# Kernel tuning notes

Hardware: AMD Instinct MI355X
Metric: run time of the kernel (lower is better)

## Reference

```python
import jax, jax.numpy as jnp
import numpy as np

LAMBDA = 0.5
WINDOW = 2
NUM_SCALES = 2
EPS = 1e-5


def setup_inputs() -> dict:
    key = jax.random.key(0)
    ks = jax.random.split(key, 9)
    N, C, T, Vw = 32, 96, 300, 50
    V = 25
    out_c = 192
    return {
        "x": jax.random.normal(ks[0], (N, C, T, Vw), jnp.float32),
        "xx": jax.random.normal(ks[1], (N, 3, 300, V), jnp.float32),
        "A_res": jax.random.normal(ks[2], (Vw, Vw), jnp.float32) * 1e-6,
        "W": jax.random.normal(ks[3], (out_c, NUM_SCALES * C), jnp.float32) * 0.05,
        "b": jax.random.normal(ks[4], (out_c,), jnp.float32) * 0.01,
        "gamma": jnp.ones((out_c,), jnp.float32),
        "beta": jnp.zeros((out_c,), jnp.float32),
        "running_mean": jax.random.normal(ks[5], (out_c,), jnp.float32) * 0.01,
        "running_var": jax.random.uniform(ks[6], (out_c,), jnp.float32, 0.5, 1.5),
    }


def reference(x, xx, A_res, W, b, gamma, beta, running_mean, running_var):
    # xx: (N, 3, 300, V) -> (N, T=300, V, C=3)
    xxp = jnp.transpose(xx, (0, 2, 3, 1))
    # pairwise squared L2 distances (norm then squared in exp == sum of squares)
    diff = xxp[:, :, :, None, :] - xxp[:, :, None, :, :]      # (N,T,V,V,3)
    dists2 = jnp.sum(diff * diff, axis=-1)                     # (N,T,V,V)
    A_dsg = jnp.exp(-dists2 / LAMBDA)
    # conv3d with (1,1,300,1,1) kernel of 1/300 == mean over the 300 frames
    A_t = jnp.mean(A_dsg, axis=1)                              # (N,V,V)
    # per-sample symmetric normalization D^-1/2 A D^-1/2
    deg = jnp.sum(A_t, axis=-1)                                # (N,V)
    dinv = deg ** -0.5
    A_norm = A_t * dinv[:, :, None] * dinv[:, None, :]
    # kron-style repeat to spatial-temporal graph (N, V*window, V*window)
    A_large = jnp.tile(A_norm, (1, WINDOW, WINDOW))
    A = A_large + A_res                                        # (N,Vw,Vw)
    # conv2d with (1,N,1,1) kernel of 1/N == mean over the batch
    A_scale = jnp.mean(A, axis=0)                              # (Vw,Vw)
    # graph conv
    agg = jnp.einsum('vu,nctu->nctv', A_scale, x)              # (N,C,T,Vw)
    N, C, T, Vw = x.shape
    Vs = Vw // NUM_SCALES
    agg = agg.reshape(N, C, T, NUM_SCALES, Vs)
    agg = jnp.transpose(agg, (0, 3, 1, 2, 4)).reshape(N, NUM_SCALES * C, T, Vs)
    # MLP: 1x1 conv + BN (activation='linear')
    out = jnp.einsum('oc,nctv->notv', W, agg) + b[None, :, None, None]
    scale = gamma * jax.lax.rsqrt(running_var + EPS)
    out = out * scale[None, :, None, None] + (beta - running_mean * scale)[None, :, None, None]
    return jax.nn.relu(out)
```

## Files before the change

### kernel.cpp

```cpp
#include <hip/hip_runtime.h>
#include <hip/hip_bf16.h>

typedef __attribute__((ext_vector_type(8))) short short8;
typedef __attribute__((ext_vector_type(4))) short short4v;
typedef __attribute__((ext_vector_type(4))) float f32x4;
typedef __attribute__((ext_vector_type(2))) float f32x2;

__device__ __forceinline__ unsigned short f2bf(float f) {
    unsigned int u = __builtin_bit_cast(unsigned int, f);
    u += 0x7fffu + ((u >> 16) & 1u);
    return (unsigned short)(u >> 16);
}
__device__ __forceinline__ short4v cvt4(float a, float b, float c, float d) {
    union { __hip_bfloat162 h[2]; short4v s; } u;
    u.h[0] = __float22bfloat162_rn(make_float2(a, b));
    u.h[1] = __float22bfloat162_rn(make_float2(c, d));
    return u.s;
}

__global__ void kA(const float* __restrict__ xx, float* __restrict__ At_part) {
    __shared__ float xs3[3][60][25];
    const int tc = blockIdx.x, n = blockIdx.y;
    const int tid = threadIdx.x;
    const float* base = xx + (size_t)n * 22500 + tc * 1500;
    for (int idx = tid; idx < 4500; idx += 256) {
        int ch = idx / 1500, rt = idx % 1500;
        xs3[ch][rt / 25][rt % 25] = base[ch * 7500 + rt];
    }
    __syncthreads();
    for (int p = tid; p < 625; p += 256) {
        int v = p / 25, u = p % 25;
        float s = 0.f;
        for (int t = 0; t < 60; ++t) {
            float dx = xs3[0][t][v] - xs3[0][t][u];
            float dy = xs3[1][t][v] - xs3[1][t][u];
            float dz = xs3[2][t][v] - xs3[2][t][u];
            s += __expf(-2.f * (dx * dx + dy * dy + dz * dz));
        }
        At_part[(size_t)(n * 5 + tc) * 625 + p] = s;
    }
}

__global__ void kB1(const float* __restrict__ At_part, float* __restrict__ Acontrib) {
    __shared__ float At[625];
    __shared__ float dinv[25];
    const int n = blockIdx.x, tid = threadIdx.x;
    for (int p = tid; p < 625; p += 256) {
        float s = 0.f;
        for (int tc = 0; tc < 5; ++tc) s += At_part[(size_t)(n * 5 + tc) * 625 + p];
        At[p] = s;
    }
    __syncthreads();
    if (tid < 25) {
        float d = 0.f;
        for (int u = 0; u < 25; ++u) d += At[tid * 25 + u];
        dinv[tid] = rsqrtf(d * (1.f / 300.f));
    }
    __syncthreads();
    for (int p = tid; p < 625; p += 256)
        Acontrib[n * 625 + p] = At[p] * (1.f / 300.f) * dinv[p / 25] * dinv[p % 25] * (1.f / 32.f);
}

__global__ void kB2(const float* __restrict__ Acontrib, const float* __restrict__ A_res,
                    const float* __restrict__ W, const float* __restrict__ b,
                    const float* __restrict__ gamma, const float* __restrict__ beta,
                    const float* __restrict__ rm, const float* __restrict__ rv,
                    short* __restrict__ bsTg, short* __restrict__ Wpg,
                    float* __restrict__ bbg) {
    const int tid = threadIdx.x;
    if (blockIdx.x == 0) {
        __shared__ float macc[625];
        for (int p = tid; p < 625; p += 256) {
            float s = 0.f;
            for (int n = 0; n < 32; ++n) s += Acontrib[n * 625 + p];
            macc[p] = s;
        }
        __syncthreads();
        for (int idx = tid; idx < 64 * 72; idx += 256) {
            int col = idx / 72, u = idx % 72;
            float v = 0.f;
            if (col < 50 && u < 50) v = macc[(col % 25) * 25 + (u % 25)] + A_res[col * 50 + u];
            bsTg[idx] = (short)f2bf(v);
        }
        if (tid < 192) {
            float sc = gamma[tid] * rsqrtf(rv[tid] + 1e-5f);
            bbg[tid] = b[tid] * sc + beta[tid] - rm[tid] * sc;
        }
    } else {
        const int e = (blockIdx.x - 1) * 1024 + tid * 4;
        const int o = e / 192;
        const float sc = gamma[o] * rsqrtf(rv[o] + 1e-5f);
        float4 w = *(const float4*)(W + e);
        short4v s4 = { (short)f2bf(w.x * sc), (short)f2bf(w.y * sc),
                       (short)f2bf(w.z * sc), (short)f2bf(w.w * sc) };
        *(short4v*)(Wpg + e) = s4;
    }
}

#define XLIM (46080000 - 2)
__device__ __forceinline__ void ldx(const float* __restrict__ x, int rowbase,
                                    int kc, f32x2 (&xr)[2][4]) {
#pragma unroll
    for (int ks = 0; ks < 2; ++ks)
#pragma unroll
        for (int h = 0; h < 4; ++h) {
            int off = rowbase + ks * 32 + kc + h * 2;
            off = off < XLIM ? off : XLIM;
            xr[ks][h] = *(const f32x2*)(x + off);
        }
}

__global__ __launch_bounds__(384, 3)
void kC(const float* __restrict__ x, const short* __restrict__ Wpg,
        const short* __restrict__ bsTg, const float* __restrict__ bbg,
        float* __restrict__ out) {
    __shared__ __align__(16) short bsT[64 * 72];
    __shared__ __align__(16) short a2T[2][32][200];

    const int tid = threadIdx.x;
    const int lane = tid & 63;
    const int wid = tid >> 6;
    const int lam = lane & 15;
    const int kc = (lane >> 4) * 8;
    const int cb = (lane >> 4) * 4;
    const int n = blockIdx.y;
    const int t0 = blockIdx.x * 4;
    const int rowb0 = n * 1440000 + (wid * 16 + lam) * 15000 + t0 * 50;

    f32x2 xr[2][4];
    ldx(x, rowb0, kc, xr);

    short8 wf[2][6];
#pragma unroll
    for (int ot = 0; ot < 2; ++ot)
#pragma unroll
        for (int ks = 0; ks < 6; ++ks)
            wf[ot][ks] = *(const short8*)(Wpg + ((2 * wid + ot) * 16 + lam) * 192 + ks * 32 + kc);

    float bb[2];
#pragma unroll
    for (int ot = 0; ot < 2; ++ot) bb[ot] = bbg[(2 * wid + ot) * 16 + lam];

    {
        const int4* src = (const int4*)bsTg;
        int4* dst = (int4*)bsT;
        for (int i = tid; i < 576; i += 384) dst[i] = src[i];
    }

    asm volatile("s_waitcnt lgkmcnt(0)" ::: "memory");
    __builtin_amdgcn_s_barrier();

    const f32x4 z = {0.f, 0.f, 0.f, 0.f};
    const int cgl = wid * 16 + lam;

#pragma unroll 1
    for (int tl = 0; tl < 4; ++tl) {
        short* a2w = &a2T[tl & 1][0][0];

        short8 xb[2];
#pragma unroll
        for (int ks = 0; ks < 2; ++ks) {
            union { short4v h[2]; short8 v; } u;
            u.h[0] = cvt4(xr[ks][0].x, xr[ks][0].y, xr[ks][1].x, xr[ks][1].y);
            u.h[1] = cvt4(xr[ks][2].x, xr[ks][2].y, xr[ks][3].x, xr[ks][3].y);
            xb[ks] = u.v;
        }
        if (tl < 3) ldx(x, rowb0 + (tl + 1) * 50, kc, xr);

        f32x4 acc1[4];
#pragma unroll
        for (int m = 0; m < 4; ++m) acc1[m] = z;
#pragma unroll
        for (int ks = 0; ks < 2; ++ks)
#pragma unroll
            for (int m = 0; m < 4; ++m) {
                const short8 af = *(const short8*)(bsT + (m * 16 + lam) * 72 + ks * 32 + kc);
                acc1[m] = __builtin_amdgcn_mfma_f32_16x16x32_bf16(af, xb[ks], acc1[m], 0, 0, 0);
            }

#pragma unroll
        for (int m = 0; m < 3; ++m) {
            short4v sv = cvt4(acc1[m][0], acc1[m][1], acc1[m][2], acc1[m][3]);
#pragma unroll
            for (int r = 0; r < 4; ++r) {
                const int v = m * 16 + cb + r;
                const int s = v >= 25;
                a2w[(v - 25 * s) * 200 + s * 96 + cgl] = sv[r];
            }
        }
        if (cb == 0) {
            a2w[23 * 200 + 96 + cgl] = (short)f2bf(acc1[3][0]);
            a2w[24 * 200 + 96 + cgl] = (short)f2bf(acc1[3][1]);
        }

        asm volatile("s_waitcnt lgkmcnt(0)" ::: "memory");
        __builtin_amdgcn_s_barrier();

        f32x4 acc2[2][2];
#pragma unroll
        for (int g = 0; g < 2; ++g) { acc2[g][0] = z; acc2[g][1] = z; }
#pragma unroll
        for (int ks = 0; ks < 6; ++ks) {
            const short8 A0 = *(const short8*)(a2w + lam * 200 + ks * 32 + kc);
            const short8 A1 = *(const short8*)(a2w + (16 + lam) * 200 + ks * 32 + kc);
#pragma unroll
            for (int ot = 0; ot < 2; ++ot) {
                acc2[0][ot] = __builtin_amdgcn_mfma_f32_16x16x32_bf16(A0, wf[ot][ks], acc2[0][ot], 0, 0, 0);
                acc2[1][ot] = __builtin_amdgcn_mfma_f32_16x16x32_bf16(A1, wf[ot][ks], acc2[1][ot], 0, 0, 0);
            }
        }

        const int t = t0 + tl;
#pragma unroll
        for (int ot = 0; ot < 2; ++ot) {
            const int o = (2 * wid + ot) * 16 + lam;
            float* op = out + ((size_t)(n * 192 + o) * 300 + t) * 25;
#pragma unroll
            for (int r = 0; r < 4; ++r) {
                float vv = acc2[0][ot][r] + bb[ot];
                op[cb + r] = vv > 0.f ? vv : 0.f;
            }
#pragma unroll
            for (int r = 0; r < 4; ++r) {
                const int tv = 16 + cb + r;
                if (tv < 25) {
                    float vv = acc2[1][ot][r] + bb[ot];
                    op[tv] = vv > 0.f ? vv : 0.f;
                }
            }
        }
    }
}

extern "C" void kernel_launch(void* const* d_in, const int* in_sizes, int n_in,
                              void* d_out, int out_size, void* d_ws, size_t ws_size,
                              hipStream_t stream) {
    const float* x     = (const float*)d_in[0];
    const float* xx    = (const float*)d_in[1];
    const float* A_res = (const float*)d_in[2];
    const float* W     = (const float*)d_in[3];
    const float* b     = (const float*)d_in[4];
    const float* gamma = (const float*)d_in[5];
    const float* beta  = (const float*)d_in[6];
    const float* rm    = (const float*)d_in[7];
    const float* rv    = (const float*)d_in[8];
    float* out = (float*)d_out;

    char* ws = (char*)d_ws;
    float* At_part  = (float*)ws;
    float* Acontrib = (float*)(ws + 400000);
    short* bsTg     = (short*)(ws + 480000);
    short* Wpg      = (short*)(ws + 489216);
    float* bbg      = (float*)(ws + 562944);

    kA<<<dim3(5, 32), 256, 0, stream>>>(xx, At_part);
    kB1<<<32, 256, 0, stream>>>(At_part, Acontrib);
    kB2<<<37, 256, 0, stream>>>(Acontrib, A_res, W, b, gamma, beta, rm, rv, bsTg, Wpg, bbg);
    kC<<<dim3(75, 32), 384, 0, stream>>>(x, Wpg, bsTg, bbg, out);
}
```

Before: 187.5 us.

## Stage x tiles through swizzled LDS with coalesced loads and double buffering

Replaces the per-lane strided 8-byte loads of x, where each lane read its own channel row, with cooperative block-wide loads that walk contiguous time/vertex runs per channel. The values are converted to bf16 and written into an XOR-swizzled, double-buffered LDS tile. The MFMA B fragments are then read from LDS, and the a2T row stride is padded from 200 to 208 to reduce bank conflicts. The intent is better global-load coalescing, at the cost of extra LDS traffic, roughly 24KB more shared memory (which may lower occupancy), and zero-fill setup work.

Result: faster. 181.5 us (-3.2%).

```diff
diff --git a/kernel.cpp b/kernel.cpp
--- a/kernel.cpp
+++ b/kernel.cpp
@@ -10,6 +10,11 @@
     unsigned int u = __builtin_bit_cast(unsigned int, f);
     u += 0x7fffu + ((u >> 16) & 1u);
     return (unsigned short)(u >> 16);
+}
+__device__ __forceinline__ unsigned int pack2(float a, float b) {
+    union { __hip_bfloat162 h; unsigned int u; } r;
+    r.h = __float22bfloat162_rn(make_float2(a, b));
+    return r.u;
 }
 __device__ __forceinline__ short4v cvt4(float a, float b, float c, float d) {
     union { __hip_bfloat162 h[2]; short4v s; } u;
@@ -97,25 +102,35 @@
     }
 }
 
-#define XLIM (46080000 - 2)
-__device__ __forceinline__ void ldx(const float* __restrict__ x, int rowbase,
-                                    int kc, f32x2 (&xr)[2][4]) {
-#pragma unroll
-    for (int ks = 0; ks < 2; ++ks)
-#pragma unroll
-        for (int h = 0; h < 4; ++h) {
-            int off = rowbase + ks * 32 + kc + h * 2;
-            off = off < XLIM ? off : XLIM;
-            xr[ks][h] = *(const f32x2*)(x + off);
-        }
+__device__ __forceinline__ void ldx(const float* __restrict__ x, int gbase,
+                                    f32x2 (&pf)[7], int tid) {
+#pragma unroll
+    for (int i = 0; i < 7; ++i) {
+        int idx = i * 384 + tid;
+        idx = idx < 2400 ? idx : 2399;
+        int c = idx / 25, q = idx - c * 25;
+        pf[i] = *(const f32x2*)(x + gbase + c * 15000 + 2 * q);
+    }
+}
+__device__ __forceinline__ void stx(char* xsb, int slot, const f32x2 (&pf)[7], int tid) {
+#pragma unroll
+    for (int i = 0; i < 7; ++i) {
+        int idx = i * 384 + tid;
+        if (idx < 2400) {
+            int c = idx / 25, q = idx - c * 25;
+            *(unsigned int*)(xsb + ((slot * 12288 + c * 128 + q * 4) ^ ((c & 7) << 4)))
+                = pack2(pf[i].x, pf[i].y);
+        }
+    }
 }
 
 __global__ __launch_bounds__(384, 3)
 void kC(const float* __restrict__ x, const short* __restrict__ Wpg,
         const short* __restrict__ bsTg, const float* __restrict__ bbg,
         float* __restrict__ out) {
+    __shared__ __align__(16) char xsb[2 * 12288];
     __shared__ __align__(16) short bsT[64 * 72];
-    __shared__ __align__(16) short a2T[2][32][200];
+    __shared__ __align__(16) short a2T[2][32][208];
 
     const int tid = threadIdx.x;
     const int lane = tid & 63;
@@ -125,10 +140,18 @@
     const int cb = (lane >> 4) * 4;
     const int n = blockIdx.y;
     const int t0 = blockIdx.x * 4;
-    const int rowb0 = n * 1440000 + (wid * 16 + lam) * 15000 + t0 * 50;
-
-    f32x2 xr[2][4];
-    ldx(x, rowb0, kc, xr);
+    const int gb0 = n * 1440000 + t0 * 50;
+    const int cgl = wid * 16 + lam;
+
+    f32x2 pf2[13];
+#pragma unroll
+    for (int i = 0; i < 13; ++i) {
+        int idx = i * 384 + tid;
+        idx = idx < 4800 ? idx : 4799;
+        int c = idx / 50, q2 = idx - c * 50;
+        int tl = q2 >= 25, q = q2 - 25 * tl;
+        pf2[i] = *(const f32x2*)(x + gb0 + c * 15000 + tl * 50 + 2 * q);
+    }
 
     short8 wf[2][6];
 #pragma unroll
@@ -146,27 +169,44 @@
         int4* dst = (int4*)bsT;
         for (int i = tid; i < 576; i += 384) dst[i] = src[i];
     }
-
+    for (int idx = tid; idx < 1344; idx += 384) {
+        int r = idx / 7, k = idx - r * 7;
+        int slot = r / 96, c = r - 96 * slot;
+        *(unsigned int*)(xsb + ((slot * 12288 + c * 128 + (50 + 2 * k) * 2) ^ ((c & 7) << 4))) = 0;
+    }
+    for (int idx = tid; idx < 1456; idx += 384) {
+        int buf = idx / 728, rem = idx - buf * 728;
+        int row = 25 + rem / 104, col2 = rem - (rem / 104) * 104;
+        *((unsigned int*)&a2T[buf][row][0] + col2) = 0;
+    }
+#pragma unroll
+    for (int i = 0; i < 13; ++i) {
+        int idx = i * 384 + tid;
+        if (idx < 4800) {
+            int c = idx / 50, q2 = idx - c * 50;
+            int tl = q2 >= 25, q = q2 - 25 * tl;
+            *(unsigned int*)(xsb + ((tl * 12288 + c * 128 + q * 4) ^ ((c & 7) << 4)))
+                = pack2(pf2[i].x, pf2[i].y);
+        }
+    }
     asm volatile("s_waitcnt lgkmcnt(0)" ::: "memory");
     __builtin_amdgcn_s_barrier();
 
     const f32x4 z = {0.f, 0.f, 0.f, 0.f};
-    const int cgl = wid * 16 + lam;
+    f32x2 pf[7];
 
 #pragma unroll 1
     for (int tl = 0; tl < 4; ++tl) {
-        short* a2w = &a2T[tl & 1][0][0];
+        const int slot = tl & 1;
+        short* a2w = &a2T[slot][0][0];
+
+        if (tl < 2) ldx(x, gb0 + (tl + 2) * 50, pf, tid);
 
         short8 xb[2];
 #pragma unroll
-        for (int ks = 0; ks < 2; ++ks) {
-            union { short4v h[2]; short8 v; } u;
-            u.h[0] = cvt4(xr[ks][0].x, xr[ks][0].y, xr[ks][1].x, xr[ks][1].y);
-            u.h[1] = cvt4(xr[ks][2].x, xr[ks][2].y, xr[ks][3].x, xr[ks][3].y);
-            xb[ks] = u.v;
-        }
-        if (tl < 3) ldx(x, rowb0 + (tl + 1) * 50, kc, xr);
-
+        for (int ks = 0; ks < 2; ++ks)
+            xb[ks] = *(const short8*)(xsb +
+                ((slot * 12288 + cgl * 128 + (ks * 32 + kc) * 2) ^ ((cgl & 7) << 4)));
         f32x4 acc1[4];
 #pragma unroll
         for (int m = 0; m < 4; ++m) acc1[m] = z;
@@ -185,12 +225,12 @@
             for (int r = 0; r < 4; ++r) {
                 const int v = m * 16 + cb + r;
                 const int s = v >= 25;
-                a2w[(v - 25 * s) * 200 + s * 96 + cgl] = sv[r];
+                a2w[(v - 25 * s) * 208 + s * 96 + cgl] = sv[r];
             }
         }
         if (cb == 0) {
-            a2w[23 * 200 + 96 + cgl] = (short)f2bf(acc1[3][0]);
-            a2w[24 * 200 + 96 + cgl] = (short)f2bf(acc1[3][1]);
+            a2w[23 * 208 + 96 + cgl] = (short)f2bf(acc1[3][0]);
+            a2w[24 * 208 + 96 + cgl] = (short)f2bf(acc1[3][1]);
         }
 
         asm volatile("s_waitcnt lgkmcnt(0)" ::: "memory");
@@ -201,14 +241,16 @@
         for (int g = 0; g < 2; ++g) { acc2[g][0] = z; acc2[g][1] = z; }
 #pragma unroll
         for (int ks = 0; ks < 6; ++ks) {
-            const short8 A0 = *(const short8*)(a2w + lam * 200 + ks * 32 + kc);
-            const short8 A1 = *(const short8*)(a2w + (16 + lam) * 200 + ks * 32 + kc);
+            const short8 A0 = *(const short8*)(a2w + lam * 208 + ks * 32 + kc);
+            const short8 A1 = *(const short8*)(a2w + (16 + lam) * 208 + ks * 32 + kc);
 #pragma unroll
             for (int ot = 0; ot < 2; ++ot) {
                 acc2[0][ot] = __builtin_amdgcn_mfma_f32_16x16x32_bf16(A0, wf[ot][ks], acc2[0][ot], 0, 0, 0);
                 acc2[1][ot] = __builtin_amdgcn_mfma_f32_16x16x32_bf16(A1, wf[ot][ks], acc2[1][ot], 0, 0, 0);
             }
         }
+
+        if (tl < 2) stx(xsb, slot, pf, tid);
 
         const int t = t0 + tl;
 #pragma unroll
```
